# Optimization experiments

Hardware: AMD Instinct MI355X
Metric: run time of the kernel (lower is better)

Reference implementation:

```python
import jax, jax.numpy as jnp
import numpy as np

ALPHA = 0.2
BETA = 1.0
TEMPERATURE = 0.05
EPS = 1e-8  # torch cosine_similarity eps


def setup_inputs() -> dict:
    key = jax.random.key(0)
    k1, k2 = jax.random.split(key)
    B, R, D = 4096, 18, 256  # rows, segment size (1 anchor + 1 pos + 16 negs), embed dim
    features = jax.random.normal(k1, (B * R, D), dtype=jnp.float32)
    scores = jax.random.normal(k2, (B * (R - 1),), dtype=jnp.float32)
    row_sizes = jnp.full((B,), R, dtype=jnp.int32)  # uniform ragged sizes
    logit_scale = jnp.array([1.0 / TEMPERATURE], dtype=jnp.float32)
    return {"features": features, "scores": scores, "row_sizes": row_sizes,
            "logit_scale": logit_scale}


def reference(features, scores, row_sizes, logit_scale):
    B = row_sizes.shape[0]
    R = features.shape[0] // B  # uniform segment size
    D = features.shape[1]
    f3 = features.reshape(B, R, D)
    anchor = f3[:, 0]          # [B, D]
    tgt = f3[:, 1:]            # [B, R-1, D]  (positive first, then negatives)

    # --- per-row cosine sims + log_softmax + KLDiv(batchmean) ---
    an = jnp.maximum(jnp.linalg.norm(anchor, axis=-1, keepdims=True), EPS)  # [B,1]
    tn = jnp.maximum(jnp.linalg.norm(tgt, axis=-1), EPS)                    # [B,R-1]
    cos = jnp.einsum('bd,bkd->bk', anchor, tgt) / (an * tn)                 # [B,R-1]
    emb_log = jax.nn.log_softmax(cos, axis=-1)                              # [B,R-1]
    ce = jax.nn.softmax(scores.reshape(B, R - 1), axis=-1)                  # [B,R-1]
    # torch KLDivLoss(reduction='batchmean') on a length-(R-1) vector divides by (R-1)
    kl = jnp.sum(ce * (jnp.log(ce) - emb_log), axis=-1) / (R - 1)           # [B]
    loss = jnp.mean(BETA * kl)

    # --- single InfoNCE over all rows: anchors vs [positives; all negatives] ---
    pos = f3[:, 1]                                   # [B, D]
    negs = f3[:, 2:].reshape(B * (R - 2), D)         # [B*(R-2), D]
    targets = jnp.concatenate([pos, negs], axis=0)   # [B*(R-1), D]
    logits = logit_scale[0] * (anchor @ targets.T)   # [B, B*(R-1)]
    labels = jnp.arange(B)
    # cross_entropy(logits, labels) with mean reduction
    infonce = jnp.mean(jax.nn.logsumexp(logits, axis=-1) - logits[labels, labels])

    return loss + ALPHA * infonce
```

## Files before the change

### kernel.cpp

```cpp
#include <hip/hip_runtime.h>
#include <math.h>

#define ALPHA 0.2f
#define BETA 1.0f
#define EPSV 1e-8f
#define LOG2E 1.4426950408889634f
#define LN2 0.6931471805599453f

#define BATCH 4096
#define RR 18
#define KT 17
#define DD 256
#define NTGT (BATCH*KT)

#define BMW 32
#define NWAVES 4
#define BMB (BMW*NWAVES)
#define MBLK (BATCH/BMB)
#define BN 64
#define NCHUNKT (NTGT/BN)
#define NSPLIT 64
#define NCHUNK (NCHUNKT/NSPLIT)
#define NSLOT (NSPLIT*2)
#define CHUNK_BYTES (BN*DD)

typedef int   i32x8  __attribute__((ext_vector_type(8)));
typedef float f32x16 __attribute__((ext_vector_type(16)));

__device__ inline void gl_lds16(const void* g, void* l){
  __builtin_amdgcn_global_load_lds(
      (const __attribute__((address_space(1))) unsigned int*)g,
      (__attribute__((address_space(3))) unsigned int*)l, 16, 0, 0);
}

__device__ inline int pk8(float a, float b, float c, float d){
  int p = __builtin_amdgcn_cvt_pk_fp8_f32(a, b, 0, false);
  return  __builtin_amdgcn_cvt_pk_fp8_f32(c, d, p, true);
}

__device__ inline i32x8 ld8_2(const unsigned char* plo, const unsigned char* phi){
  uint4 lo = *(const uint4*)plo, hi = *(const uint4*)phi;
  return (i32x8){(int)lo.x,(int)lo.y,(int)lo.z,(int)lo.w,
                 (int)hi.x,(int)hi.y,(int)hi.z,(int)hi.w};
}


__global__ __launch_bounds__(256) void tconv_kernel(
    const float* __restrict__ feat, const float* __restrict__ lscale,
    unsigned char* __restrict__ abf8, unsigned char* __restrict__ tbf8,
    float* __restrict__ carr, float* __restrict__ diag){
  int c = blockIdx.x, tid = threadIdx.x;
  int r = tid >> 2, q = tid & 3;
  int t = c*64 + r;
  unsigned tb = (unsigned)t / 17u;
  unsigned tk = (unsigned)t - tb*17u;
  const float* trow = feat + ((size_t)tb*RR + tk + 1)*DD;
  const float* arow = feat + (size_t)tb*RR*DD;
  float d = 0.f, qq = 0.f, asq = 0.f;
  unsigned pkv[16];
  #pragma unroll
  for (int i=0;i<16;++i){
    float4 tv = ((const float4*)trow)[q + 4*i];
    float4 av = ((const float4*)arow)[q + 4*i];
    d   += av.x*tv.x + av.y*tv.y + av.z*tv.z + av.w*tv.w;
    qq  += tv.x*tv.x + tv.y*tv.y + tv.z*tv.z + tv.w*tv.w;
    asq += av.x*av.x + av.y*av.y + av.z*av.z + av.w*av.w;
    pkv[i] = (unsigned)pk8(tv.x, tv.y, tv.z, tv.w);
  }
  int m = r & 31, mt = r >> 5;
  size_t cb = (size_t)c*CHUNK_BYTES;
  #pragma unroll
  for (int i=0;i<16;++i){
    int ki = i >> 2, hf = (i >> 1) & 1, w = i & 1;
    *(unsigned*)(tbf8 + cb + (size_t)((ki*2+mt)*2+w)*1024 + hf*512 + m*16 + q*4)
        = pkv[i];
  }
  d   += __shfl_xor(d,1);   d   += __shfl_xor(d,2);
  qq  += __shfl_xor(qq,1);  qq  += __shfl_xor(qq,2);
  asq += __shfl_xor(asq,1); asq += __shfl_xor(asq,2);
  if (q == 0){
    float an = fmaxf(sqrtf(asq), EPSV), tn = fmaxf(sqrtf(qq), EPSV);
    carr[t] = d / (an*tn);
    if (tk == 0) diag[tb] = d;
  }
  if (c < 256){
    int a = tid >> 4, j = tid & 15;
    int b = c*16 + a;
    const float* ar = feat + (size_t)b*RR*DD + j*16;
    float s2 = lscale[0]*LOG2E;
    unsigned o0, o1, o2, o3;
    { float4 v=((const float4*)ar)[0]; o0=(unsigned)pk8(v.x*s2,v.y*s2,v.z*s2,v.w*s2); }
    { float4 v=((const float4*)ar)[1]; o1=(unsigned)pk8(v.x*s2,v.y*s2,v.z*s2,v.w*s2); }
    { float4 v=((const float4*)ar)[2]; o2=(unsigned)pk8(v.x*s2,v.y*s2,v.z*s2,v.w*s2); }
    { float4 v=((const float4*)ar)[3]; o3=(unsigned)pk8(v.x*s2,v.y*s2,v.z*s2,v.w*s2); }
    *(uint4*)(abf8 + (size_t)b*DD + j*16) = make_uint4(o0,o1,o2,o3);
  }
}

__global__ __launch_bounds__(256,4) void gemm_lse_kernel(
    const unsigned char* __restrict__ abf8, const unsigned char* __restrict__ tbf8,
    float* __restrict__ part_m, float* __restrict__ part_s){
  __shared__ __align__(16) unsigned char Bs[2][CHUNK_BYTES];
  const int tid = threadIdx.x, lane = tid & 63, wave = tid >> 6;
  const int mb = blockIdx.y, ns = blockIdx.x;
  const int l31 = lane & 31, half = lane >> 5;

  const char* gbase = (const char*)tbf8 + (size_t)(ns*NCHUNK)*CHUNK_BYTES;
  auto stage = [&](int ch){
    const char* g = gbase + (size_t)ch*CHUNK_BYTES;
    char* l = (char*)Bs[ch & 1];
    #pragma unroll
    for (int j=0;j<4;++j){
      int off = j*4096 + tid*16;
      gl_lds16(g + off, l + off);
    }
  };
  stage(0);

  i32x8 af[4];
  {
    const unsigned char* ab = abf8
        + (size_t)(mb*BMB + wave*BMW + l31)*DD + half*32;
    #pragma unroll
    for (int ki=0;ki<4;++ki)
      af[ki] = ld8_2(ab + ki*64, ab + ki*64 + 16);
  }

  float run_m = -INFINITY, run_s = 0.f;

  for (int ch=0; ch<NCHUNK; ++ch){
    __syncthreads();
    if (ch+1 < NCHUNK) stage(ch+1);
    const unsigned char* frag = &Bs[ch&1][0] + lane*16;

    f32x16 a0 = (f32x16)(0.f), a1 = (f32x16)(0.f);
    #pragma unroll
    for (int ki=0; ki<4; ++ki){
      i32x8 tf0 = ld8_2(frag + (size_t)(ki*4+0)*1024, frag + (size_t)(ki*4+1)*1024);
      i32x8 tf1 = ld8_2(frag + (size_t)(ki*4+2)*1024, frag + (size_t)(ki*4+3)*1024);
      a0 = __builtin_amdgcn_mfma_scale_f32_32x32x64_f8f6f4(tf0, af[ki], a0, 0,0, 0,127, 0,127);
      a1 = __builtin_amdgcn_mfma_scale_f32_32x32x64_f8f6f4(tf1, af[ki], a1, 0,0, 0,127, 0,127);
    }

    f32x16 tm = __builtin_elementwise_max(a0, a1);
    float m8[8];
    #pragma unroll
    for (int i=0;i<8;++i) m8[i] = fmaxf(tm[i], tm[i+8]);
    float mx = fmaxf(fmaxf(fmaxf(m8[0],m8[1]),fmaxf(m8[2],m8[3])),
                     fmaxf(fmaxf(m8[4],m8[5]),fmaxf(m8[6],m8[7])));
    f32x16 e;
    #pragma unroll
    for (int i=0;i<16;++i)
      e[i] = __builtin_amdgcn_exp2f(a0[i]-mx) + __builtin_amdgcn_exp2f(a1[i]-mx);
    float s8[8];
    #pragma unroll
    for (int i=0;i<8;++i) s8[i] = e[i] + e[i+8];
    float sh = ((s8[0]+s8[1])+(s8[2]+s8[3]))+((s8[4]+s8[5])+(s8[6]+s8[7]));
    float nm = fmaxf(run_m, mx);
    run_s = run_s*__builtin_amdgcn_exp2f(run_m-nm)
          + sh*__builtin_amdgcn_exp2f(mx-nm);
    run_m = nm;
  }

  int gm = mb*BMB + wave*BMW + l31;
  int slot = ns*2 + half;
  part_m[(size_t)gm*NSLOT + slot] = run_m;
  part_s[(size_t)gm*NSLOT + slot] = run_s;
}

__global__ __launch_bounds__(256) void combine_kernel(
    const float* __restrict__ part_m, const float* __restrict__ part_s,
    const float* __restrict__ diag, const float* __restrict__ carr,
    const float* __restrict__ scores, const float* __restrict__ lscale,
    float* __restrict__ outarr){
  int lane = threadIdx.x & 63, wv = threadIdx.x >> 6;
  int b = blockIdx.x*4 + wv;
  float s = lscale[0];
  const float* pm = part_m + (size_t)b*NSLOT;
  const float* ps = part_s + (size_t)b*NSLOT;
  float m0 = pm[lane], m1 = pm[lane+64];
  float v0 = ps[lane], v1 = ps[lane+64];
  float M = fmaxf(m0, m1);
  #pragma unroll
  for (int off=1; off<64; off<<=1) M = fmaxf(M, __shfl_xor(M, off));
  float S = v0*__builtin_amdgcn_exp2f(m0-M) + v1*__builtin_amdgcn_exp2f(m1-M);
  #pragma unroll
  for (int off=1; off<64; off<<=1) S += __shfl_xor(S, off);
  float inf = (M + __log2f(S))*LN2 - s*diag[b];

  const float* cb = carr + (size_t)b*KT;
  const float* sb = scores + (size_t)b*KT;
  float cv[KT], sw[KT];
  #pragma unroll
  for (int j=0;j<KT;++j){ cv[j] = cb[j]; sw[j] = sb[j]; }
  float cm = -INFINITY, sm = -INFINITY;
  #pragma unroll
  for (int j=0;j<KT;++j){ cm = fmaxf(cm, cv[j]); sm = fmaxf(sm, sw[j]); }
  float cs = 0.f, ss = 0.f;
  #pragma unroll
  for (int j=0;j<KT;++j){
    cs += __builtin_amdgcn_exp2f((cv[j]-cm)*LOG2E);
    ss += __builtin_amdgcn_exp2f((sw[j]-sm)*LOG2E);
  }
  float lse_c = cm + __logf(cs);
  float lse_s = sm + __logf(ss);
  float kl = 0.f;
  #pragma unroll
  for (int j=0;j<KT;++j){
    float lq = sw[j] - lse_s;
    float lp = cv[j] - lse_c;
    kl += __builtin_amdgcn_exp2f(lq*LOG2E)*(lq - lp);
  }
  kl *= (1.0f/KT);
  if (lane == 0) outarr[b] = BETA*kl + ALPHA*inf;
}

__global__ __launch_bounds__(256) void final_kernel(
    const float* __restrict__ outarr, float* __restrict__ out){
  __shared__ float sh[4];
  int tid = threadIdx.x, lane = tid & 63, wv = tid >> 6;
  float v = 0.f;
  for (int i = tid; i < BATCH; i += 256) v += outarr[i];
  #pragma unroll
  for (int off=1; off<64; off<<=1) v += __shfl_xor(v, off);
  if (lane == 0) sh[wv] = v;
  __syncthreads();
  if (tid == 0) out[0] = (sh[0]+sh[1]+sh[2]+sh[3])*(1.0f/BATCH);
}

extern "C" void kernel_launch(void* const* d_in, const int* in_sizes, int n_in,
                              void* d_out, int out_size, void* d_ws, size_t ws_size,
                              hipStream_t stream){
  const float* feat   = (const float*)d_in[0];
  const float* scores = (const float*)d_in[1];
  const float* lscale = (const float*)d_in[3];

  float* ws     = (float*)d_ws;
  float* diag   = ws;
  float* outarr = diag + BATCH;
  float* carr   = outarr + BATCH;
  float* part_m = carr + NTGT;
  float* part_s = part_m + (size_t)BATCH*NSLOT;
  unsigned char* abf8 = (unsigned char*)(part_s + (size_t)BATCH*NSLOT);
  unsigned char* tbf8 = abf8 + (size_t)BATCH*DD;

  tconv_kernel<<<NCHUNKT, 256, 0, stream>>>(feat, lscale, abf8, tbf8, carr, diag);
  gemm_lse_kernel<<<dim3(NSPLIT, MBLK), 256, 0, stream>>>(abf8, tbf8, part_m, part_s);
  combine_kernel<<<BATCH/4, 256, 0, stream>>>(part_m, part_s, diag, carr, scores,
                                              lscale, outarr);
  final_kernel<<<1, 256, 0, stream>>>(outarr, (float*)d_out);
}
```

Before: 199.8 us.

## Retile GEMM waves as 2x2 grid sharing B fragments across two anchor tiles

Each wave now covers 64 anchor rows by 32 target columns instead of 32 rows by 64 columns. Every LDS-loaded target fragment therefore feeds two MFMAs, and LDS read traffic per MFMA is halved. The cost is twice the A-fragment registers, separate online log-sum-exp state per tile, and twice as many partial slots for the combine kernel to reduce. Launch bounds drop from 4 to 3 blocks per SIMD to leave room for the extra registers.

Result: slower. 207.0 us (+3.6%).

```diff
diff --git a/kernel.cpp b/kernel.cpp
--- a/kernel.cpp
+++ b/kernel.cpp
@@ -13,15 +13,13 @@
 #define DD 256
 #define NTGT (BATCH*KT)
 
-#define BMW 32
-#define NWAVES 4
-#define BMB (BMW*NWAVES)
+#define BMB 128
 #define MBLK (BATCH/BMB)
 #define BN 64
 #define NCHUNKT (NTGT/BN)
 #define NSPLIT 64
 #define NCHUNK (NCHUNKT/NSPLIT)
-#define NSLOT (NSPLIT*2)
+#define NSLOT (NSPLIT*4)
 #define CHUNK_BYTES (BN*DD)
 
 typedef int   i32x8  __attribute__((ext_vector_type(8)));
@@ -97,13 +95,14 @@
   }
 }
 
-__global__ __launch_bounds__(256,4) void gemm_lse_kernel(
+__global__ __launch_bounds__(256,3) void gemm_lse_kernel(
     const unsigned char* __restrict__ abf8, const unsigned char* __restrict__ tbf8,
     float* __restrict__ part_m, float* __restrict__ part_s){
   __shared__ __align__(16) unsigned char Bs[2][CHUNK_BYTES];
   const int tid = threadIdx.x, lane = tid & 63, wave = tid >> 6;
   const int mb = blockIdx.y, ns = blockIdx.x;
   const int l31 = lane & 31, half = lane >> 5;
+  const int ap = wave >> 1, mt = wave & 1;
 
   const char* gbase = (const char*)tbf8 + (size_t)(ns*NCHUNK)*CHUNK_BYTES;
   auto stage = [&](int ch){
@@ -117,16 +116,20 @@
   };
   stage(0);
 
-  i32x8 af[4];
+  i32x8 af[2][4];
   {
-    const unsigned char* ab = abf8
-        + (size_t)(mb*BMB + wave*BMW + l31)*DD + half*32;
-    #pragma unroll
-    for (int ki=0;ki<4;++ki)
-      af[ki] = ld8_2(ab + ki*64, ab + ki*64 + 16);
-  }
-
-  float run_m = -INFINITY, run_s = 0.f;
+    #pragma unroll
+    for (int nt=0;nt<2;++nt){
+      const unsigned char* ab = abf8
+          + (size_t)(mb*BMB + ap*64 + nt*32 + l31)*DD + half*32;
+      #pragma unroll
+      for (int ki=0;ki<4;++ki)
+        af[nt][ki] = ld8_2(ab + ki*64, ab + ki*64 + 16);
+    }
+  }
+
+  float run_m[2] = {-INFINITY,-INFINITY};
+  float run_s[2] = {0.f,0.f};
 
   for (int ch=0; ch<NCHUNK; ++ch){
     __syncthreads();
@@ -136,36 +139,41 @@
     f32x16 a0 = (f32x16)(0.f), a1 = (f32x16)(0.f);
     #pragma unroll
     for (int ki=0; ki<4; ++ki){
-      i32x8 tf0 = ld8_2(frag + (size_t)(ki*4+0)*1024, frag + (size_t)(ki*4+1)*1024);
-      i32x8 tf1 = ld8_2(frag + (size_t)(ki*4+2)*1024, frag + (size_t)(ki*4+3)*1024);
-      a0 = __builtin_amdgcn_mfma_scale_f32_32x32x64_f8f6f4(tf0, af[ki], a0, 0,0, 0,127, 0,127);
-      a1 = __builtin_amdgcn_mfma_scale_f32_32x32x64_f8f6f4(tf1, af[ki], a1, 0,0, 0,127, 0,127);
-    }
-
-    f32x16 tm = __builtin_elementwise_max(a0, a1);
-    float m8[8];
-    #pragma unroll
-    for (int i=0;i<8;++i) m8[i] = fmaxf(tm[i], tm[i+8]);
-    float mx = fmaxf(fmaxf(fmaxf(m8[0],m8[1]),fmaxf(m8[2],m8[3])),
-                     fmaxf(fmaxf(m8[4],m8[5]),fmaxf(m8[6],m8[7])));
-    f32x16 e;
-    #pragma unroll
-    for (int i=0;i<16;++i)
-      e[i] = __builtin_amdgcn_exp2f(a0[i]-mx) + __builtin_amdgcn_exp2f(a1[i]-mx);
-    float s8[8];
-    #pragma unroll
-    for (int i=0;i<8;++i) s8[i] = e[i] + e[i+8];
-    float sh = ((s8[0]+s8[1])+(s8[2]+s8[3]))+((s8[4]+s8[5])+(s8[6]+s8[7]));
-    float nm = fmaxf(run_m, mx);
-    run_s = run_s*__builtin_amdgcn_exp2f(run_m-nm)
-          + sh*__builtin_amdgcn_exp2f(mx-nm);
-    run_m = nm;
-  }
-
-  int gm = mb*BMB + wave*BMW + l31;
-  int slot = ns*2 + half;
-  part_m[(size_t)gm*NSLOT + slot] = run_m;
-  part_s[(size_t)gm*NSLOT + slot] = run_s;
+      i32x8 tf = ld8_2(frag + (size_t)((ki*2+mt)*2+0)*1024,
+                       frag + (size_t)((ki*2+mt)*2+1)*1024);
+      a0 = __builtin_amdgcn_mfma_scale_f32_32x32x64_f8f6f4(tf, af[0][ki], a0, 0,0, 0,127, 0,127);
+      a1 = __builtin_amdgcn_mfma_scale_f32_32x32x64_f8f6f4(tf, af[1][ki], a1, 0,0, 0,127, 0,127);
+    }
+
+    #pragma unroll
+    for (int nt=0; nt<2; ++nt){
+      const f32x16& a = nt ? a1 : a0;
+      float m8[8];
+      #pragma unroll
+      for (int i=0;i<8;++i) m8[i] = fmaxf(a[i], a[i+8]);
+      float mx = fmaxf(fmaxf(fmaxf(m8[0],m8[1]),fmaxf(m8[2],m8[3])),
+                       fmaxf(fmaxf(m8[4],m8[5]),fmaxf(m8[6],m8[7])));
+      f32x16 e;
+      #pragma unroll
+      for (int i=0;i<16;++i) e[i] = __builtin_amdgcn_exp2f(a[i]-mx);
+      float s8[8];
+      #pragma unroll
+      for (int i=0;i<8;++i) s8[i] = e[i] + e[i+8];
+      float sh = ((s8[0]+s8[1])+(s8[2]+s8[3]))+((s8[4]+s8[5])+(s8[6]+s8[7]));
+      float nm = fmaxf(run_m[nt], mx);
+      run_s[nt] = run_s[nt]*__builtin_amdgcn_exp2f(run_m[nt]-nm)
+                + sh*__builtin_amdgcn_exp2f(mx-nm);
+      run_m[nt] = nm;
+    }
+  }
+
+  #pragma unroll
+  for (int nt=0; nt<2; ++nt){
+    int gm = mb*BMB + ap*64 + nt*32 + l31;
+    int slot = ns*4 + mt*2 + half;
+    part_m[(size_t)gm*NSLOT + slot] = run_m[nt];
+    part_s[(size_t)gm*NSLOT + slot] = run_s[nt];
+  }
 }
 
 __global__ __launch_bounds__(256) void combine_kernel(
@@ -178,12 +186,15 @@
   float s = lscale[0];
   const float* pm = part_m + (size_t)b*NSLOT;
   const float* ps = part_s + (size_t)b*NSLOT;
-  float m0 = pm[lane], m1 = pm[lane+64];
-  float v0 = ps[lane], v1 = ps[lane+64];
-  float M = fmaxf(m0, m1);
+  float mv[4], sv[4];
+  #pragma unroll
+  for (int i=0;i<4;++i){ mv[i] = pm[lane+i*64]; sv[i] = ps[lane+i*64]; }
+  float M = fmaxf(fmaxf(mv[0],mv[1]), fmaxf(mv[2],mv[3]));
   #pragma unroll
   for (int off=1; off<64; off<<=1) M = fmaxf(M, __shfl_xor(M, off));
-  float S = v0*__builtin_amdgcn_exp2f(m0-M) + v1*__builtin_amdgcn_exp2f(m1-M);
+  float S = 0.f;
+  #pragma unroll
+  for (int i=0;i<4;++i) S += sv[i]*__builtin_amdgcn_exp2f(mv[i]-M);
   #pragma unroll
   for (int off=1; off<64; off<<=1) S += __shfl_xor(S, off);
   float inf = (M + __log2f(S))*LN2 - s*diag[b];
```

## Fuse pipeline into cooperative persistent kernel with atomic task scheduling

Applied to the files above, without the earlier changes.

Replaces the four separate launches with one cooperative kernel on 512 blocks. It runs the fp8 conversion, a dynamically scheduled GEMM+logsumexp phase fed by an atomic counter, the per-row combine and the final reduction, separated by grid-wide syncs. NSPLIT grows from 64 to 136, so each task covers fewer chunks and load balances more finely, and the combine step now reduces more partial slots. The goal is to remove launch gaps and tail imbalance, at the cost of grid-sync overhead and lower occupancy (launch bounds 3 instead of 4). If the cooperative launch fails, it falls back to the multi-kernel path.

New measurement: 413.2 us. 2.07x slower.

```diff
diff --git a/kernel.cpp b/kernel.cpp
--- a/kernel.cpp
+++ b/kernel.cpp
@@ -1,5 +1,8 @@
 #include <hip/hip_runtime.h>
+#include <hip/hip_cooperative_groups.h>
 #include <math.h>
+
+namespace cg = cooperative_groups;
 
 #define ALPHA 0.2f
 #define BETA 1.0f
@@ -14,15 +17,16 @@
 #define NTGT (BATCH*KT)
 
 #define BMW 32
-#define NWAVES 4
-#define BMB (BMW*NWAVES)
+#define BMB 128
 #define MBLK (BATCH/BMB)
 #define BN 64
 #define NCHUNKT (NTGT/BN)
-#define NSPLIT 64
+#define NSPLIT 136
 #define NCHUNK (NCHUNKT/NSPLIT)
+#define NTASK (MBLK*NSPLIT)
 #define NSLOT (NSPLIT*2)
 #define CHUNK_BYTES (BN*DD)
+#define GRID 512
 
 typedef int   i32x8  __attribute__((ext_vector_type(8)));
 typedef float f32x16 __attribute__((ext_vector_type(16)));
@@ -45,11 +49,10 @@
 }
 
 
-__global__ __launch_bounds__(256) void tconv_kernel(
-    const float* __restrict__ feat, const float* __restrict__ lscale,
-    unsigned char* __restrict__ abf8, unsigned char* __restrict__ tbf8,
-    float* __restrict__ carr, float* __restrict__ diag){
-  int c = blockIdx.x, tid = threadIdx.x;
+__device__ __forceinline__ void conv_chunk(
+    int c, int tid, const float* __restrict__ feat,
+    unsigned char* __restrict__ tbf8, float* __restrict__ carr,
+    float* __restrict__ diag){
   int r = tid >> 2, q = tid & 3;
   int t = c*64 + r;
   unsigned tb = (unsigned)t / 17u;
@@ -83,40 +86,37 @@
     carr[t] = d / (an*tn);
     if (tk == 0) diag[tb] = d;
   }
-  if (c < 256){
-    int a = tid >> 4, j = tid & 15;
-    int b = c*16 + a;
-    const float* ar = feat + (size_t)b*RR*DD + j*16;
-    float s2 = lscale[0]*LOG2E;
-    unsigned o0, o1, o2, o3;
-    { float4 v=((const float4*)ar)[0]; o0=(unsigned)pk8(v.x*s2,v.y*s2,v.z*s2,v.w*s2); }
-    { float4 v=((const float4*)ar)[1]; o1=(unsigned)pk8(v.x*s2,v.y*s2,v.z*s2,v.w*s2); }
-    { float4 v=((const float4*)ar)[2]; o2=(unsigned)pk8(v.x*s2,v.y*s2,v.z*s2,v.w*s2); }
-    { float4 v=((const float4*)ar)[3]; o3=(unsigned)pk8(v.x*s2,v.y*s2,v.z*s2,v.w*s2); }
-    *(uint4*)(abf8 + (size_t)b*DD + j*16) = make_uint4(o0,o1,o2,o3);
-  }
-}
-
-__global__ __launch_bounds__(256,4) void gemm_lse_kernel(
+}
+
+__device__ __forceinline__ void conv_anchor(
+    int blk, int tid, const float* __restrict__ feat, float s2,
+    unsigned char* __restrict__ abf8){
+  int a = tid >> 4, j = tid & 15;
+  int b = blk*16 + a;
+  const float* ar = feat + (size_t)b*RR*DD + j*16;
+  unsigned o0,o1,o2,o3;
+  { float4 v=((const float4*)ar)[0]; o0=(unsigned)pk8(v.x*s2,v.y*s2,v.z*s2,v.w*s2); }
+  { float4 v=((const float4*)ar)[1]; o1=(unsigned)pk8(v.x*s2,v.y*s2,v.z*s2,v.w*s2); }
+  { float4 v=((const float4*)ar)[2]; o2=(unsigned)pk8(v.x*s2,v.y*s2,v.z*s2,v.w*s2); }
+  { float4 v=((const float4*)ar)[3]; o3=(unsigned)pk8(v.x*s2,v.y*s2,v.z*s2,v.w*s2); }
+  *(uint4*)(abf8 + (size_t)b*DD + j*16) = make_uint4(o0,o1,o2,o3);
+}
+
+__device__ __forceinline__ void gemm_task(
+    int mb, int ns, int tid,
     const unsigned char* __restrict__ abf8, const unsigned char* __restrict__ tbf8,
-    float* __restrict__ part_m, float* __restrict__ part_s){
-  __shared__ __align__(16) unsigned char Bs[2][CHUNK_BYTES];
-  const int tid = threadIdx.x, lane = tid & 63, wave = tid >> 6;
-  const int mb = blockIdx.y, ns = blockIdx.x;
+    float* __restrict__ part_m, float* __restrict__ part_s,
+    unsigned char (*Bs)[CHUNK_BYTES]){
+  const int lane = tid & 63, wave = tid >> 6;
   const int l31 = lane & 31, half = lane >> 5;
-
   const char* gbase = (const char*)tbf8 + (size_t)(ns*NCHUNK)*CHUNK_BYTES;
-  auto stage = [&](int ch){
-    const char* g = gbase + (size_t)ch*CHUNK_BYTES;
-    char* l = (char*)Bs[ch & 1];
-    #pragma unroll
-    for (int j=0;j<4;++j){
-      int off = j*4096 + tid*16;
-      gl_lds16(g + off, l + off);
-    }
-  };
-  stage(0);
-
+
+  {
+    const char* g = gbase;
+    char* l = (char*)Bs[0];
+    #pragma unroll
+    for (int j=0;j<4;++j) gl_lds16(g + j*4096 + tid*16, l + j*4096 + tid*16);
+  }
   i32x8 af[4];
   {
     const unsigned char* ab = abf8
@@ -127,17 +127,23 @@
   }
 
   float run_m = -INFINITY, run_s = 0.f;
-
   for (int ch=0; ch<NCHUNK; ++ch){
     __syncthreads();
-    if (ch+1 < NCHUNK) stage(ch+1);
+    if (ch+1 < NCHUNK){
+      const char* g = gbase + (size_t)(ch+1)*CHUNK_BYTES;
+      char* l = (char*)Bs[(ch+1) & 1];
+      #pragma unroll
+      for (int j=0;j<4;++j) gl_lds16(g + j*4096 + tid*16, l + j*4096 + tid*16);
+    }
     const unsigned char* frag = &Bs[ch&1][0] + lane*16;
 
     f32x16 a0 = (f32x16)(0.f), a1 = (f32x16)(0.f);
     #pragma unroll
     for (int ki=0; ki<4; ++ki){
-      i32x8 tf0 = ld8_2(frag + (size_t)(ki*4+0)*1024, frag + (size_t)(ki*4+1)*1024);
-      i32x8 tf1 = ld8_2(frag + (size_t)(ki*4+2)*1024, frag + (size_t)(ki*4+3)*1024);
+      i32x8 tf0 = ld8_2(frag + (size_t)((ki*2+0)*2+0)*1024,
+                        frag + (size_t)((ki*2+0)*2+1)*1024);
+      i32x8 tf1 = ld8_2(frag + (size_t)((ki*2+1)*2+0)*1024,
+                        frag + (size_t)((ki*2+1)*2+1)*1024);
       a0 = __builtin_amdgcn_mfma_scale_f32_32x32x64_f8f6f4(tf0, af[ki], a0, 0,0, 0,127, 0,127);
       a1 = __builtin_amdgcn_mfma_scale_f32_32x32x64_f8f6f4(tf1, af[ki], a1, 0,0, 0,127, 0,127);
     }
@@ -168,51 +174,133 @@
   part_s[(size_t)gm*NSLOT + slot] = run_s;
 }
 
+__device__ __forceinline__ void combine_b(
+    int b, int lane,
+    const float* __restrict__ part_m, const float* __restrict__ part_s,
+    const float* __restrict__ diag, const float* __restrict__ carr,
+    const float* __restrict__ scores, float s, float* __restrict__ outarr){
+  const float* pm = part_m + (size_t)b*NSLOT;
+  const float* ps = part_s + (size_t)b*NSLOT;
+  float mv[5], sv[5];
+  float M = -INFINITY;
+  #pragma unroll
+  for (int i=0;i<5;++i){
+    int idx = lane + i*64;
+    bool ok = (idx < NSLOT);
+    mv[i] = ok ? pm[idx] : -INFINITY;
+    sv[i] = ok ? ps[idx] : 0.f;
+    M = fmaxf(M, mv[i]);
+  }
+  #pragma unroll
+  for (int off=1; off<64; off<<=1) M = fmaxf(M, __shfl_xor(M,off));
+  float S = 0.f;
+  #pragma unroll
+  for (int i=0;i<5;++i) S += sv[i]*__builtin_amdgcn_exp2f(mv[i]-M);
+  #pragma unroll
+  for (int off=1; off<64; off<<=1) S += __shfl_xor(S,off);
+  float inf_ = (M + __log2f(S))*LN2 - s*diag[b];
+
+  const float* cb = carr + (size_t)b*KT;
+  const float* sb = scores + (size_t)b*KT;
+  float cv[KT], sw[KT];
+  #pragma unroll
+  for (int j=0;j<KT;++j){ cv[j] = cb[j]; sw[j] = sb[j]; }
+  float cm = -INFINITY, sm = -INFINITY;
+  #pragma unroll
+  for (int j=0;j<KT;++j){ cm = fmaxf(cm, cv[j]); sm = fmaxf(sm, sw[j]); }
+  float cs = 0.f, ss = 0.f;
+  #pragma unroll
+  for (int j=0;j<KT;++j){
+    cs += __builtin_amdgcn_exp2f((cv[j]-cm)*LOG2E);
+    ss += __builtin_amdgcn_exp2f((sw[j]-sm)*LOG2E);
+  }
+  float lse_c = cm + __logf(cs);
+  float lse_s = sm + __logf(ss);
+  float kl = 0.f;
+  #pragma unroll
+  for (int j=0;j<KT;++j){
+    float lq = sw[j] - lse_s;
+    float lp = cv[j] - lse_c;
+    kl += __builtin_amdgcn_exp2f(lq*LOG2E)*(lq - lp);
+  }
+  kl *= (1.0f/KT);
+  if (lane == 0) outarr[b] = BETA*kl + ALPHA*inf_;
+}
+
+__global__ __launch_bounds__(256,3) void mega_kernel(
+    const float* __restrict__ feat, const float* __restrict__ scores,
+    const float* __restrict__ lscale,
+    int* __restrict__ ctr, float* __restrict__ diag, float* __restrict__ outarr,
+    float* __restrict__ carr, float* __restrict__ part_m, float* __restrict__ part_s,
+    unsigned char* __restrict__ abf8, unsigned char* __restrict__ tbf8,
+    float* __restrict__ out){
+  __shared__ __align__(16) unsigned char Bs[2][CHUNK_BYTES];
+  __shared__ int stask;
+  __shared__ float shf[4];
+  cg::grid_group grid = cg::this_grid();
+  const int tid = threadIdx.x, lane = tid & 63, wave = tid >> 6;
+  const int bid = blockIdx.x;
+
+  for (int c = bid; c < NCHUNKT; c += GRID)
+    conv_chunk(c, tid, feat, tbf8, carr, diag);
+  if (bid < 256) conv_anchor(bid, tid, feat, lscale[0]*LOG2E, abf8);
+  if (bid == 0 && tid == 0) *ctr = 0;
+  grid.sync();
+
+  while (true){
+    __syncthreads();
+    if (tid == 0) stask = atomicAdd(ctr, 1);
+    __syncthreads();
+    int t = stask;
+    if (t >= NTASK) break;
+    unsigned mb = (unsigned)t / (unsigned)NSPLIT;
+    int ns = t - (int)mb*NSPLIT;
+    gemm_task((int)mb, ns, tid, abf8, tbf8, part_m, part_s, Bs);
+  }
+  grid.sync();
+
+  {
+    float s = lscale[0];
+    for (int b = bid*4 + wave; b < BATCH; b += GRID*4)
+      combine_b(b, lane, part_m, part_s, diag, carr, scores, s, outarr);
+  }
+  grid.sync();
+
+  if (bid == 0){
+    float v = 0.f;
+    for (int i = tid; i < BATCH; i += 256) v += outarr[i];
+    #pragma unroll
+    for (int off=1; off<64; off<<=1) v += __shfl_xor(v, off);
+    if (lane == 0) shf[wave] = v;
+    __syncthreads();
+    if (tid == 0) out[0] = (shf[0]+shf[1]+shf[2]+shf[3])*(1.0f/BATCH);
+  }
+}
+
+__global__ __launch_bounds__(256) void tconv_kernel(
+    const float* __restrict__ feat, const float* __restrict__ lscale,
+    unsigned char* __restrict__ abf8, unsigned char* __restrict__ tbf8,
+    float* __restrict__ carr, float* __restrict__ diag){
+  conv_chunk(blockIdx.x, threadIdx.x, feat, tbf8, carr, diag);
+  if (blockIdx.x < 256)
+    conv_anchor(blockIdx.x, threadIdx.x, feat, lscale[0]*LOG2E, abf8);
+}
+
+__global__ __launch_bounds__(256,3) void gemm_kernel(
+    const unsigned char* __restrict__ abf8, const unsigned char* __restrict__ tbf8,
+    float* __restrict__ part_m, float* __restrict__ part_s){
+  __shared__ __align__(16) unsigned char Bs[2][CHUNK_BYTES];
+  gemm_task(blockIdx.y, blockIdx.x, threadIdx.x, abf8, tbf8, part_m, part_s, Bs);
+}
+
 __global__ __launch_bounds__(256) void combine_kernel(
     const float* __restrict__ part_m, const float* __restrict__ part_s,
     const float* __restrict__ diag, const float* __restrict__ carr,
     const float* __restrict__ scores, const float* __restrict__ lscale,
     float* __restrict__ outarr){
-  int lane = threadIdx.x & 63, wv = threadIdx.x >> 6;
-  int b = blockIdx.x*4 + wv;
-  float s = lscale[0];
-  const float* pm = part_m + (size_t)b*NSLOT;
-  const float* ps = part_s + (size_t)b*NSLOT;
-  float m0 = pm[lane], m1 = pm[lane+64];
-  float v0 = ps[lane], v1 = ps[lane+64];
-  float M = fmaxf(m0, m1);
-  #pragma unroll
-  for (int off=1; off<64; off<<=1) M = fmaxf(M, __shfl_xor(M, off));
-  float S = v0*__builtin_amdgcn_exp2f(m0-M) + v1*__builtin_amdgcn_exp2f(m1-M);
-  #pragma unroll
-  for (int off=1; off<64; off<<=1) S += __shfl_xor(S, off);
-  float inf = (M + __log2f(S))*LN2 - s*diag[b];
-
-  const float* cb = carr + (size_t)b*KT;
-  const float* sb = scores + (size_t)b*KT;
-  float cv[KT], sw[KT];
-  #pragma unroll
-  for (int j=0;j<KT;++j){ cv[j] = cb[j]; sw[j] = sb[j]; }
-  float cm = -INFINITY, sm = -INFINITY;
-  #pragma unroll
-  for (int j=0;j<KT;++j){ cm = fmaxf(cm, cv[j]); sm = fmaxf(sm, sw[j]); }
-  float cs = 0.f, ss = 0.f;
-  #pragma unroll
-  for (int j=0;j<KT;++j){
-    cs += __builtin_amdgcn_exp2f((cv[j]-cm)*LOG2E);
-    ss += __builtin_amdgcn_exp2f((sw[j]-sm)*LOG2E);
-  }
-  float lse_c = cm + __logf(cs);
-  float lse_s = sm + __logf(ss);
-  float kl = 0.f;
-  #pragma unroll
-  for (int j=0;j<KT;++j){
-    float lq = sw[j] - lse_s;
-    float lp = cv[j] - lse_c;
-    kl += __builtin_amdgcn_exp2f(lq*LOG2E)*(lq - lp);
-  }
-  kl *= (1.0f/KT);
-  if (lane == 0) outarr[b] = BETA*kl + ALPHA*inf;
+  int b = blockIdx.x*4 + (threadIdx.x >> 6);
+  combine_b(b, threadIdx.x & 63, part_m, part_s, diag, carr, scores,
+            lscale[0], outarr);
 }
 
 __global__ __launch_bounds__(256) void final_kernel(
@@ -235,18 +323,29 @@
   const float* scores = (const float*)d_in[1];
   const float* lscale = (const float*)d_in[3];
 
-  float* ws     = (float*)d_ws;
-  float* diag   = ws;
+  int*   ctr    = (int*)d_ws;
+  float* diag   = (float*)d_ws + 16;
   float* outarr = diag + BATCH;
   float* carr   = outarr + BATCH;
   float* part_m = carr + NTGT;
   float* part_s = part_m + (size_t)BATCH*NSLOT;
   unsigned char* abf8 = (unsigned char*)(part_s + (size_t)BATCH*NSLOT);
   unsigned char* tbf8 = abf8 + (size_t)BATCH*DD;
-
-  tconv_kernel<<<NCHUNKT, 256, 0, stream>>>(feat, lscale, abf8, tbf8, carr, diag);
-  gemm_lse_kernel<<<dim3(NSPLIT, MBLK), 256, 0, stream>>>(abf8, tbf8, part_m, part_s);
-  combine_kernel<<<BATCH/4, 256, 0, stream>>>(part_m, part_s, diag, carr, scores,
-                                              lscale, outarr);
-  final_kernel<<<1, 256, 0, stream>>>(outarr, (float*)d_out);
-}
+  float* outp = (float*)d_out;
+
+  void* args[] = { (void*)&feat, (void*)&scores, (void*)&lscale,
+                   (void*)&ctr, (void*)&diag, (void*)&outarr, (void*)&carr,
+                   (void*)&part_m, (void*)&part_s, (void*)&abf8, (void*)&tbf8,
+                   (void*)&outp };
+  hipError_t err = hipLaunchCooperativeKernel((const void*)mega_kernel,
+                                              dim3(GRID), dim3(256),
+                                              args, 0, stream);
+  if (err != hipSuccess){
+    (void)hipGetLastError();
+    tconv_kernel<<<NCHUNKT, 256, 0, stream>>>(feat, lscale, abf8, tbf8, carr, diag);
+    gemm_kernel<<<dim3(NSPLIT, MBLK), 256, 0, stream>>>(abf8, tbf8, part_m, part_s);
+    combine_kernel<<<BATCH/4, 256, 0, stream>>>(part_m, part_s, diag, carr,
+                                                scores, lscale, outarr);
+    final_kernel<<<1, 256, 0, stream>>>(outarr, (float*)d_out);
+  }
+}
```
